# Kernel optimization log

Measured on AMD Instinct MI355X. Metric: run time of the kernel, lower is better.

The kernel has to match this reference:

```python
import jax, jax.numpy as jnp
import numpy as np

N = 100000      # nodes
E = 3200000     # edges
IN_DIM = 128
HID = 128
OUT_DIM = 1
LAYERS = 8
ALPHA = 0.1
THETA = 0.5


def setup_inputs() -> dict:
    key = jax.random.key(0)
    ks = jax.random.split(key, 8)
    x = jax.random.normal(ks[0], (N, IN_DIM), dtype=jnp.float32)
    edge_index = jax.random.randint(ks[1], (2, E), 0, N, dtype=jnp.int64)
    edge_weight = jax.random.uniform(ks[2], (E,), dtype=jnp.float32)  # unused by original forward path
    W_in = jax.random.normal(ks[3], (IN_DIM, HID), dtype=jnp.float32) * 0.05
    b_in = jnp.zeros((HID,), dtype=jnp.float32)
    W_gcn = jax.random.normal(ks[4], (LAYERS, HID, HID), dtype=jnp.float32) * 0.05
    W_out = jax.random.normal(ks[5], (HID, OUT_DIM), dtype=jnp.float32) * 0.05
    b_out = jnp.zeros((OUT_DIM,), dtype=jnp.float32)
    return {"x": x, "edge_weight": edge_weight, "W_in": W_in, "b_in": b_in,
            "W_gcn": W_gcn, "W_out": W_out, "b_out": b_out, "edge_index": edge_index}


def _gcn_norm(edge_index, dtype):
    # add self loops (fill value 1), symmetric normalization deg^-1/2 A deg^-1/2
    sl = jnp.arange(N, dtype=edge_index.dtype)
    row = jnp.concatenate([edge_index[0], sl])
    col = jnp.concatenate([edge_index[1], sl])
    w = jnp.ones(row.shape[0], dtype=dtype)
    deg = jax.ops.segment_sum(w, col, num_segments=N)
    dinv = jnp.where(deg > 0, jax.lax.rsqrt(deg), 0.0)
    norm = dinv[row] * dinv[col]
    return row, col, norm


def reference(x, edge_weight, W_in, b_in, W_gcn, W_out, b_out, edge_index):
    row, col, norm = _gcn_norm(edge_index, x.dtype)
    h = x @ W_in + b_in            # initial_proj
    h0 = h                          # residual x0
    for i in range(LAYERS):
        # dropout is identity in eval mode
        msg = h[row] * norm[:, None]                       # gather + scale [E+N, HID]
        agg = jax.ops.segment_sum(msg, col, num_segments=N)
        s = (1.0 - ALPHA) * agg + ALPHA * h0               # identity-mapped residual
        beta = float(np.log(THETA / (i + 1) + 1.0))
        h = (1.0 - beta) * s + beta * (s @ W_gcn[i])       # GCNII weight mix
        h = jax.nn.relu(h)
    return h @ W_out + b_out
```

## Files before the change

kernel.cpp:

```cpp
#include <hip/hip_runtime.h>
#include <hip/hip_bf16.h>
#include <math.h>

#define N_NODES 100000
#define N_EDGES 3200000
#define HID 128
#define LAYERS 8
#define ALPHA 0.1f
#define THETA 0.5f

#define SCAN_TILE 1024
#define NB_SCAN ((N_NODES + SCAN_TILE - 1) / SCAN_TILE)

typedef unsigned int uint;
typedef unsigned short ushort;
typedef __attribute__((ext_vector_type(8))) short short8;
typedef __attribute__((ext_vector_type(4))) float f32x4;

__device__ inline float bf_lo(uint p) { return __uint_as_float(p << 16); }
__device__ inline float bf_hi(uint p) { return __uint_as_float(p & 0xffff0000u); }
__device__ inline uint bf_pack(float x, float y) {
    uint ux = __float_as_uint(x), uy = __float_as_uint(y);
    uint rx = (ux + 0x7fffu + ((ux >> 16) & 1u)) >> 16;
    uint ry = (uy + 0x7fffu + ((uy >> 16) & 1u)) >> 16;
    return rx | (ry << 16);
}
__device__ inline ushort bfr(float x) {
    uint u = __float_as_uint(x);
    return (ushort)((u + 0x7fffu + ((u >> 16) & 1u)) >> 16);
}
__device__ inline float bff(ushort s) { return __uint_as_float(((uint)s) << 16); }

__device__ inline float rec_w(uint k) { return __uint_as_float((k >> 17) << 16); }

__global__ __launch_bounds__(256) void k_count(const int* __restrict__ col,
                                               int* __restrict__ cnt) {
    int e = blockIdx.x * 256 + threadIdx.x;
    if (e < N_EDGES) atomicAdd(&cnt[col[e]], 1);
}

__global__ __launch_bounds__(256) void k_dinv(const int* __restrict__ cnt,
                                              float* __restrict__ dinv) {
    int n = blockIdx.x * 256 + threadIdx.x;
    if (n < N_NODES) dinv[n] = rsqrtf((float)(cnt[n] + 1));
}

__global__ __launch_bounds__(256) void k_scan1(const int* __restrict__ cnt,
                                               int* __restrict__ indptr,
                                               int* __restrict__ bsum) {
    __shared__ int lds[256];
    int t = threadIdx.x;
    int base = blockIdx.x * SCAN_TILE + t * 4;
    int v[4];
    int s = 0;
#pragma unroll
    for (int j = 0; j < 4; ++j) {
        v[j] = (base + j < N_NODES) ? cnt[base + j] : 0;
        s += v[j];
    }
    lds[t] = s;
    __syncthreads();
    for (int off = 1; off < 256; off <<= 1) {
        int u = (t >= off) ? lds[t - off] : 0;
        __syncthreads();
        lds[t] += u;
        __syncthreads();
    }
    int run = lds[t] - s;
#pragma unroll
    for (int j = 0; j < 4; ++j) {
        if (base + j < N_NODES) indptr[base + j] = run;
        run += v[j];
    }
    if (t == 255) bsum[blockIdx.x] = lds[255];
}

__global__ __launch_bounds__(256) void k_scan2(const int* __restrict__ bsum,
                                               int* __restrict__ boff) {
    __shared__ int lds[256];
    int t = threadIdx.x;
    int v = (t < NB_SCAN) ? bsum[t] : 0;
    lds[t] = v;
    __syncthreads();
    for (int off = 1; off < 256; off <<= 1) {
        int u = (t >= off) ? lds[t - off] : 0;
        __syncthreads();
        lds[t] += u;
        __syncthreads();
    }
    boff[t] = lds[t] - v;
}

__global__ __launch_bounds__(256) void k_scan3(int* __restrict__ indptr,
                                               const int* __restrict__ boff) {
    int base = blockIdx.x * SCAN_TILE + threadIdx.x * 4;
    int add = boff[blockIdx.x];
#pragma unroll
    for (int j = 0; j < 4; ++j) {
        if (base + j < N_NODES) indptr[base + j] += add;
    }
    if (blockIdx.x == 0 && threadIdx.x == 0) indptr[N_NODES] = N_EDGES;
}

__global__ __launch_bounds__(256) void k_fill(const int* __restrict__ rowi,
                                              const int* __restrict__ coli,
                                              const float* __restrict__ dinv,
                                              const int* __restrict__ indptr,
                                              int* __restrict__ cursor,
                                              uint* __restrict__ csr4) {
    int e = blockIdx.x * 256 + threadIdx.x;
    if (e >= N_EDGES) return;
    int r = rowi[e];
    int c = coli[e];
    int p = indptr[c] + atomicAdd(&cursor[c], 1);
    float nrm = dinv[r] * dinv[c];
    csr4[p] = (uint)r | ((uint)bfr(nrm) << 17);
}

__global__ __launch_bounds__(256) void k_wprep(const float* __restrict__ Wg,
                                               ushort* __restrict__ Wt) {
    int l = blockIdx.x;
    const float* W = Wg + (size_t)l * HID * HID;
    ushort* T = Wt + (size_t)l * HID * HID;
    int t = threadIdx.x;
#pragma unroll
    for (int i = 0; i < 16; ++i) {
        int idx = t + 256 * i;
        int k = idx >> 5;
        int c4 = idx & 31;
        float4 v = *(const float4*)(W + (size_t)k * HID + c4 * 4);
        T[(c4 * 4 + 0) * HID + k] = bfr(v.x);
        T[(c4 * 4 + 1) * HID + k] = bfr(v.y);
        T[(c4 * 4 + 2) * HID + k] = bfr(v.z);
        T[(c4 * 4 + 3) * HID + k] = bfr(v.w);
    }
}

#define TN 32
#define SAS 136

__global__ __launch_bounds__(256) void k_layer(const uint* __restrict__ h,
                                               const uint* __restrict__ h0,
                                               const float* __restrict__ dinv,
                                               const int* __restrict__ indptr,
                                               const uint* __restrict__ csr4,
                                               const ushort* __restrict__ Wt,
                                               uint* __restrict__ hOut,
                                               float beta) {
    __shared__ ushort sA[TN * SAS];
    int t = threadIdx.x;
    int lane = t & 63;
    int wv = t >> 6;
    int nb = blockIdx.x * TN;

    for (int i = 0; i < 8; ++i) {
        int row = wv * 8 + i;
        int node = nb + row;
        int beg = indptr[node];
        int end = indptr[node + 1];
        float di = dinv[node];
        uint hs = h[node * 64 + lane];
        uint h0v = h0[node * 64 + lane];
        float ax[8], ay[8];
#pragma unroll
        for (int j = 0; j < 8; ++j) { ax[j] = 0.f; ay[j] = 0.f; }
        int e = beg;
        for (; e + 16 <= end; e += 16) {
            uint kk[16];
#pragma unroll
            for (int j = 0; j < 16; ++j) kk[j] = csr4[e + j];
            uint p[16];
#pragma unroll
            for (int j = 0; j < 16; ++j) p[j] = h[(kk[j] & 0x1FFFF) * 64 + lane];
#pragma unroll
            for (int j = 0; j < 16; ++j) {
                float w = rec_w(kk[j]);
                ax[j & 7] = fmaf(w, bf_lo(p[j]), ax[j & 7]);
                ay[j & 7] = fmaf(w, bf_hi(p[j]), ay[j & 7]);
            }
        }
        for (; e < end; e += 4) {
            uint kk[4];
            float w[4];
#pragma unroll
            for (int j = 0; j < 4; ++j) {
                int idx = e + j;
                kk[j] = csr4[idx < end ? idx : beg];
                w[j] = (idx < end) ? rec_w(kk[j]) : 0.f;
            }
            uint p[4];
#pragma unroll
            for (int j = 0; j < 4; ++j) p[j] = h[(kk[j] & 0x1FFFF) * 64 + lane];
#pragma unroll
            for (int j = 0; j < 4; ++j) {
                ax[j] = fmaf(w[j], bf_lo(p[j]), ax[j]);
                ay[j] = fmaf(w[j], bf_hi(p[j]), ay[j]);
            }
        }
        float sum0 = ((ax[0] + ax[1]) + (ax[2] + ax[3])) + ((ax[4] + ax[5]) + (ax[6] + ax[7]));
        float sum1 = ((ay[0] + ay[1]) + (ay[2] + ay[3])) + ((ay[4] + ay[5]) + (ay[6] + ay[7]));
        float selfw = di * di;
        float rx = (1.0f - ALPHA) * fmaf(selfw, bf_lo(hs), sum0) + ALPHA * bf_lo(h0v);
        float ry = (1.0f - ALPHA) * fmaf(selfw, bf_hi(hs), sum1) + ALPHA * bf_hi(h0v);
        *((uint*)(sA + row * SAS) + lane) = bf_pack(rx, ry);
    }
    __syncthreads();

    int fr = lane & 15;
    int fq = lane >> 4;
    f32x4 acc[2][2] = {};
#pragma unroll
    for (int kc = 0; kc < 4; ++kc) {
        int kof = kc * 32 + fq * 8;
        short8 b0 = *(const short8*)(Wt + (size_t)(wv * 32 + fr) * HID + kof);
        short8 b1 = *(const short8*)(Wt + (size_t)(wv * 32 + 16 + fr) * HID + kof);
#pragma unroll
        for (int tm = 0; tm < 2; ++tm) {
            short8 a = *(const short8*)(sA + (tm * 16 + fr) * SAS + kof);
            acc[tm][0] = __builtin_amdgcn_mfma_f32_16x16x32_bf16(a, b0, acc[tm][0], 0, 0, 0);
            acc[tm][1] = __builtin_amdgcn_mfma_f32_16x16x32_bf16(a, b1, acc[tm][1], 0, 0, 0);
        }
    }
    __syncthreads();

    float ob = 1.0f - beta;
#pragma unroll
    for (int tm = 0; tm < 2; ++tm)
#pragma unroll
        for (int tn = 0; tn < 2; ++tn)
#pragma unroll
            for (int r = 0; r < 4; ++r) {
                int row = tm * 16 + fq * 4 + r;
                int col = wv * 32 + tn * 16 + fr;
                float sv = bff(sA[row * SAS + col]);
                float val = fmaxf(fmaf(ob, sv, beta * acc[tm][tn][r]), 0.f);
                sA[row * SAS + col] = bfr(val);
            }
    __syncthreads();
#pragma unroll
    for (int i = 0; i < 2; ++i) {
        int idx = t + 256 * i;
        int r = idx >> 4;
        int q = idx & 15;
        *(uint4*)(hOut + (size_t)(nb + r) * 64 + q * 4) =
            *(const uint4*)((const uint*)(sA + r * SAS) + q * 4);
    }
}

__global__ __launch_bounds__(256) void k_gemm_in(const float* __restrict__ A,
                                                 const float* __restrict__ W,
                                                 const float* __restrict__ bias,
                                                 uint* __restrict__ out0,
                                                 uint* __restrict__ out1) {
    __shared__ float sT[32 * 64];
    __shared__ float Ws[32 * 128];
    int t = threadIdx.x;
    int tr = t & 15;
    int tc = t >> 4;
    int rowBase = blockIdx.x * 64;
    float acc[4][8] = {};

    for (int ko = 0; ko < HID; ko += 32) {
#pragma unroll
        for (int pass = 0; pass < 2; ++pass) {
            int lin = t + 256 * pass;
            int r = lin >> 3;
            int kq = lin & 7;
            int ar = rowBase + r;
            if (ar >= N_NODES) ar = N_NODES - 1;
            float4 v = *(const float4*)(A + (size_t)ar * HID + ko + 4 * kq);
            sT[(4 * kq + 0) * 64 + r] = v.x;
            sT[(4 * kq + 1) * 64 + r] = v.y;
            sT[(4 * kq + 2) * 64 + r] = v.z;
            sT[(4 * kq + 3) * 64 + r] = v.w;
        }
#pragma unroll
        for (int pass = 0; pass < 4; ++pass) {
            int lin = t + 256 * pass;
            int k = lin >> 5;
            int c4 = lin & 31;
            *(float4*)&Ws[k * 128 + 4 * c4] =
                *(const float4*)(W + (size_t)(ko + k) * HID + 4 * c4);
        }
        __syncthreads();
#pragma unroll
        for (int k = 0; k < 32; ++k) {
            float4 a = *(const float4*)&sT[k * 64 + 4 * tr];
            float4 w0 = *(const float4*)&Ws[k * 128 + 8 * tc];
            float4 w1 = *(const float4*)&Ws[k * 128 + 8 * tc + 4];
            float av[4] = {a.x, a.y, a.z, a.w};
            float wv[8] = {w0.x, w0.y, w0.z, w0.w, w1.x, w1.y, w1.z, w1.w};
#pragma unroll
            for (int i = 0; i < 4; ++i)
#pragma unroll
                for (int j = 0; j < 8; ++j)
                    acc[i][j] = fmaf(av[i], wv[j], acc[i][j]);
        }
        __syncthreads();
    }

    int c0 = 8 * tc;
    float bb[8];
#pragma unroll
    for (int j = 0; j < 8; ++j) bb[j] = bias[c0 + j];
#pragma unroll
    for (int i = 0; i < 4; ++i) {
        int r = rowBase + 4 * tr + i;
        if (r >= N_NODES) break;
        float v[8];
#pragma unroll
        for (int j = 0; j < 8; ++j) v[j] = acc[i][j] + bb[j];
        uint4 o;
        o.x = bf_pack(v[0], v[1]);
        o.y = bf_pack(v[2], v[3]);
        o.z = bf_pack(v[4], v[5]);
        o.w = bf_pack(v[6], v[7]);
        *(uint4*)(out0 + (size_t)r * 64 + c0 / 2) = o;
        *(uint4*)(out1 + (size_t)r * 64 + c0 / 2) = o;
    }
}

__global__ __launch_bounds__(256) void k_out(const uint* __restrict__ h,
                                             const float* __restrict__ W_out,
                                             const float* __restrict__ b_out,
                                             float* __restrict__ out) {
    int node = blockIdx.x * 4 + (threadIdx.x >> 6);
    if (node >= N_NODES) return;
    int lane = threadIdx.x & 63;
    uint p = h[node * 64 + lane];
    float2 wv = *(const float2*)(W_out + lane * 2);
    float pr = bf_lo(p) * wv.x + bf_hi(p) * wv.y;
#pragma unroll
    for (int off = 32; off > 0; off >>= 1) pr += __shfl_down(pr, off);
    if (lane == 0) out[node] = pr + b_out[0];
}

extern "C" void kernel_launch(void* const* d_in, const int* in_sizes, int n_in,
                              void* d_out, int out_size, void* d_ws, size_t ws_size,
                              hipStream_t stream) {
    const float* x     = (const float*)d_in[0];
    const float* W_in  = (const float*)d_in[2];
    const float* b_in  = (const float*)d_in[3];
    const float* W_gcn = (const float*)d_in[4];
    const float* W_out = (const float*)d_in[5];
    const float* b_out = (const float*)d_in[6];
    const int*   ei    = (const int*)d_in[7];
    const int* rowi = ei;
    const int* coli = ei + N_EDGES;
    float* out = (float*)d_out;

    char* ws = (char*)d_ws;
    auto alloc = [&](size_t bytes) -> char* {
        char* p = ws;
        ws += (bytes + 255) & ~(size_t)255;
        return p;
    };
    int*    cnt     = (int*)   alloc((size_t)N_NODES * 4);
    float*  dinv    = (float*) alloc((size_t)N_NODES * 4);
    int*    indptr  = (int*)   alloc((size_t)(N_NODES + 1) * 4);
    int*    cursor  = (int*)   alloc((size_t)N_NODES * 4);
    int*    bsum    = (int*)   alloc(1024 * 4);
    int*    boff    = (int*)   alloc(1024 * 4);
    uint*   csr4    = (uint*)  alloc((size_t)N_EDGES * 4);
    ushort* Wt      = (ushort*)alloc((size_t)LAYERS * HID * HID * 2);
    uint*   hA      = (uint*)  alloc((size_t)N_NODES * 64 * 4);
    uint*   hB      = (uint*)  alloc((size_t)N_NODES * 64 * 4);
    uint*   h0      = (uint*)  alloc((size_t)N_NODES * 64 * 4);

    hipMemsetAsync(cnt, 0, (size_t)N_NODES * 4, stream);
    hipMemsetAsync(cursor, 0, (size_t)N_NODES * 4, stream);

    k_count<<<(N_EDGES + 255) / 256, 256, 0, stream>>>(coli, cnt);
    k_dinv<<<(N_NODES + 255) / 256, 256, 0, stream>>>(cnt, dinv);
    k_scan1<<<NB_SCAN, 256, 0, stream>>>(cnt, indptr, bsum);
    k_scan2<<<1, 256, 0, stream>>>(bsum, boff);
    k_scan3<<<NB_SCAN, 256, 0, stream>>>(indptr, boff);
    k_fill<<<(N_EDGES + 255) / 256, 256, 0, stream>>>(rowi, coli, dinv, indptr,
                                                      cursor, csr4);
    k_wprep<<<LAYERS, 256, 0, stream>>>(W_gcn, Wt);

    k_gemm_in<<<(N_NODES + 63) / 64, 256, 0, stream>>>(x, W_in, b_in, h0, hA);

    int layer_blocks = N_NODES / TN;
    for (int l = 0; l < LAYERS; ++l) {
        const uint* hin = (l & 1) ? hB : hA;
        uint* hout      = (l & 1) ? hA : hB;
        float beta = logf(THETA / (float)(l + 1) + 1.0f);
        k_layer<<<layer_blocks, 256, 0, stream>>>(hin, h0, dinv, indptr, csr4,
                                                  Wt + (size_t)l * HID * HID,
                                                  hout, beta);
    }
    k_out<<<(N_NODES + 3) / 4, 256, 0, stream>>>(hA, W_out, b_out, out);
}
```

Measured before the change: 1.621 ms.

## Bucket CSR edges by source-node range and gather chunk-by-chunk across a wave's nodes

The CSR fill now runs as 8 passes, each covering one range of 12,500 source nodes, so each destination's neighbor list is sorted by source chunk. Per-chunk boundaries are snapshotted into a new array. The layer kernel walks the chunks in order and processes all 8 of a wave's nodes within each chunk before moving on, so concurrent gathers from h hit a narrower address range and should reuse cache better. The cost is 8 extra full edge-list passes plus snapshots in preprocessing, and many short inner loops per node that use the 4-wide tail path instead of the previous 16-wide unrolled loop.

Measured after the change: 2.043 ms. +26.1%, slower.

```diff
diff --git a/kernel.cpp b/kernel.cpp
--- a/kernel.cpp
+++ b/kernel.cpp
@@ -8,6 +8,9 @@
 #define LAYERS 8
 #define ALPHA 0.1f
 #define THETA 0.5f
+
+#define CH 8
+#define CHDIV 12500
 
 #define SCAN_TILE 1024
 #define NB_SCAN ((N_NODES + SCAN_TILE - 1) / SCAN_TILE)
@@ -102,17 +105,24 @@
     if (blockIdx.x == 0 && threadIdx.x == 0) indptr[N_NODES] = N_EDGES;
 }
 
-__global__ __launch_bounds__(256) void k_fill(const int* __restrict__ rowi,
-                                              const int* __restrict__ coli,
-                                              const float* __restrict__ dinv,
-                                              const int* __restrict__ indptr,
-                                              int* __restrict__ cursor,
-                                              uint* __restrict__ csr4) {
+__global__ __launch_bounds__(256) void k_snap(const int* __restrict__ src,
+                                              int* __restrict__ dst) {
+    int n = blockIdx.x * 256 + threadIdx.x;
+    if (n < N_NODES) dst[n] = src[n];
+}
+
+__global__ __launch_bounds__(256) void k_fill_pass(const int* __restrict__ rowi,
+                                                   const int* __restrict__ coli,
+                                                   const float* __restrict__ dinv,
+                                                   int* __restrict__ cursor,
+                                                   uint* __restrict__ csr4,
+                                                   int lo, int hi) {
     int e = blockIdx.x * 256 + threadIdx.x;
     if (e >= N_EDGES) return;
     int r = rowi[e];
+    if (r < lo || r >= hi) return;
     int c = coli[e];
-    int p = indptr[c] + atomicAdd(&cursor[c], 1);
+    int p = atomicAdd(&cursor[c], 1);
     float nrm = dinv[r] * dinv[c];
     csr4[p] = (uint)r | ((uint)bfr(nrm) << 17);
 }
@@ -143,6 +153,7 @@
                                                const uint* __restrict__ h0,
                                                const float* __restrict__ dinv,
                                                const int* __restrict__ indptr,
+                                               const int* __restrict__ bnd,
                                                const uint* __restrict__ csr4,
                                                const ushort* __restrict__ Wt,
                                                uint* __restrict__ hOut,
@@ -152,57 +163,52 @@
     int lane = t & 63;
     int wv = t >> 6;
     int nb = blockIdx.x * TN;
-
+    int myN = nb + wv * 8;
+
+    int bend = bnd[(lane & 7) * N_NODES + myN + (lane >> 3)];
+    int ip0 = indptr[myN + (lane & 7)];
+
+    float accx[8] = {0.f, 0.f, 0.f, 0.f, 0.f, 0.f, 0.f, 0.f};
+    float accy[8] = {0.f, 0.f, 0.f, 0.f, 0.f, 0.f, 0.f, 0.f};
+
+    for (int p = 0; p < CH; ++p) {
+#pragma unroll
+        for (int i = 0; i < 8; ++i) {
+            int end = __builtin_amdgcn_readlane(bend, i * 8 + p);
+            int beg = (p == 0) ? __builtin_amdgcn_readlane(ip0, i)
+                               : __builtin_amdgcn_readlane(bend, i * 8 + p - 1);
+            for (int e = beg; e < end; e += 4) {
+                uint kk[4];
+                float w[4];
+#pragma unroll
+                for (int j = 0; j < 4; ++j) {
+                    int idx = e + j;
+                    kk[j] = csr4[idx < end ? idx : beg];
+                    w[j] = (idx < end) ? rec_w(kk[j]) : 0.f;
+                }
+                uint pv[4];
+#pragma unroll
+                for (int j = 0; j < 4; ++j)
+                    pv[j] = h[(kk[j] & 0x1FFFF) * 64 + lane];
+#pragma unroll
+                for (int j = 0; j < 4; ++j) {
+                    accx[i] = fmaf(w[j], bf_lo(pv[j]), accx[i]);
+                    accy[i] = fmaf(w[j], bf_hi(pv[j]), accy[i]);
+                }
+            }
+        }
+    }
+
+#pragma unroll
     for (int i = 0; i < 8; ++i) {
-        int row = wv * 8 + i;
-        int node = nb + row;
-        int beg = indptr[node];
-        int end = indptr[node + 1];
+        int node = myN + i;
         float di = dinv[node];
         uint hs = h[node * 64 + lane];
         uint h0v = h0[node * 64 + lane];
-        float ax[8], ay[8];
-#pragma unroll
-        for (int j = 0; j < 8; ++j) { ax[j] = 0.f; ay[j] = 0.f; }
-        int e = beg;
-        for (; e + 16 <= end; e += 16) {
-            uint kk[16];
-#pragma unroll
-            for (int j = 0; j < 16; ++j) kk[j] = csr4[e + j];
-            uint p[16];
-#pragma unroll
-            for (int j = 0; j < 16; ++j) p[j] = h[(kk[j] & 0x1FFFF) * 64 + lane];
-#pragma unroll
-            for (int j = 0; j < 16; ++j) {
-                float w = rec_w(kk[j]);
-                ax[j & 7] = fmaf(w, bf_lo(p[j]), ax[j & 7]);
-                ay[j & 7] = fmaf(w, bf_hi(p[j]), ay[j & 7]);
-            }
-        }
-        for (; e < end; e += 4) {
-            uint kk[4];
-            float w[4];
-#pragma unroll
-            for (int j = 0; j < 4; ++j) {
-                int idx = e + j;
-                kk[j] = csr4[idx < end ? idx : beg];
-                w[j] = (idx < end) ? rec_w(kk[j]) : 0.f;
-            }
-            uint p[4];
-#pragma unroll
-            for (int j = 0; j < 4; ++j) p[j] = h[(kk[j] & 0x1FFFF) * 64 + lane];
-#pragma unroll
-            for (int j = 0; j < 4; ++j) {
-                ax[j] = fmaf(w[j], bf_lo(p[j]), ax[j]);
-                ay[j] = fmaf(w[j], bf_hi(p[j]), ay[j]);
-            }
-        }
-        float sum0 = ((ax[0] + ax[1]) + (ax[2] + ax[3])) + ((ax[4] + ax[5]) + (ax[6] + ax[7]));
-        float sum1 = ((ay[0] + ay[1]) + (ay[2] + ay[3])) + ((ay[4] + ay[5]) + (ay[6] + ay[7]));
         float selfw = di * di;
-        float rx = (1.0f - ALPHA) * fmaf(selfw, bf_lo(hs), sum0) + ALPHA * bf_lo(h0v);
-        float ry = (1.0f - ALPHA) * fmaf(selfw, bf_hi(hs), sum1) + ALPHA * bf_hi(h0v);
-        *((uint*)(sA + row * SAS) + lane) = bf_pack(rx, ry);
+        float rx = (1.0f - ALPHA) * fmaf(selfw, bf_lo(hs), accx[i]) + ALPHA * bf_lo(h0v);
+        float ry = (1.0f - ALPHA) * fmaf(selfw, bf_hi(hs), accy[i]) + ALPHA * bf_hi(h0v);
+        *((uint*)(sA + (wv * 8 + i) * SAS) + lane) = bf_pack(rx, ry);
     }
     __syncthreads();
 
@@ -359,6 +365,7 @@
     float*  dinv    = (float*) alloc((size_t)N_NODES * 4);
     int*    indptr  = (int*)   alloc((size_t)(N_NODES + 1) * 4);
     int*    cursor  = (int*)   alloc((size_t)N_NODES * 4);
+    int*    bnd     = (int*)   alloc((size_t)CH * N_NODES * 4);
     int*    bsum    = (int*)   alloc(1024 * 4);
     int*    boff    = (int*)   alloc(1024 * 4);
     uint*   csr4    = (uint*)  alloc((size_t)N_EDGES * 4);
@@ -368,15 +375,22 @@
     uint*   h0      = (uint*)  alloc((size_t)N_NODES * 64 * 4);
 
     hipMemsetAsync(cnt, 0, (size_t)N_NODES * 4, stream);
-    hipMemsetAsync(cursor, 0, (size_t)N_NODES * 4, stream);
-
-    k_count<<<(N_EDGES + 255) / 256, 256, 0, stream>>>(coli, cnt);
-    k_dinv<<<(N_NODES + 255) / 256, 256, 0, stream>>>(cnt, dinv);
+
+    int nblk = (N_NODES + 255) / 256;
+    int eblk = (N_EDGES + 255) / 256;
+
+    k_count<<<eblk, 256, 0, stream>>>(coli, cnt);
+    k_dinv<<<nblk, 256, 0, stream>>>(cnt, dinv);
     k_scan1<<<NB_SCAN, 256, 0, stream>>>(cnt, indptr, bsum);
     k_scan2<<<1, 256, 0, stream>>>(bsum, boff);
     k_scan3<<<NB_SCAN, 256, 0, stream>>>(indptr, boff);
-    k_fill<<<(N_EDGES + 255) / 256, 256, 0, stream>>>(rowi, coli, dinv, indptr,
-                                                      cursor, csr4);
+
+    k_snap<<<nblk, 256, 0, stream>>>(indptr, cursor);
+    for (int p = 0; p < CH; ++p) {
+        k_fill_pass<<<eblk, 256, 0, stream>>>(rowi, coli, dinv, cursor, csr4,
+                                              p * CHDIV, (p + 1) * CHDIV);
+        k_snap<<<nblk, 256, 0, stream>>>(cursor, bnd + (size_t)p * N_NODES);
+    }
     k_wprep<<<LAYERS, 256, 0, stream>>>(W_gcn, Wt);
 
     k_gemm_in<<<(N_NODES + 63) / 64, 256, 0, stream>>>(x, W_in, b_in, h0, hA);
@@ -386,7 +400,8 @@
         const uint* hin = (l & 1) ? hB : hA;
         uint* hout      = (l & 1) ? hA : hB;
         float beta = logf(THETA / (float)(l + 1) + 1.0f);
-        k_layer<<<layer_blocks, 256, 0, stream>>>(hin, h0, dinv, indptr, csr4,
+        k_layer<<<layer_blocks, 256, 0, stream>>>(hin, h0, dinv, indptr, bnd,
+                                                  csr4,
                                                   Wt + (size_t)l * HID * HID,
                                                   hout, beta);
     }
```

## Build CSR via two-pass bucketed binning instead of per-edge global atomics

Applied to the files above, without the earlier changes.

Replaces the single CSR fill kernel, which did one global atomic per edge on per-node cursors and scattered randomly, with a two-level scheme. Edges are first binned into 128-node buckets, each split into 8 sub-streams to spread atomic contention. A per-bucket kernel then places edges using LDS atomics, so final CSR writes land in a localized range. This adds an extra pass over the edges, a single-block bucket scan and a 12.8MB staging buffer.

Result: slower. 1.825 ms (+12.6%).

```diff
diff --git a/kernel.cpp b/kernel.cpp
--- a/kernel.cpp
+++ b/kernel.cpp
@@ -11,6 +11,11 @@
 
 #define SCAN_TILE 1024
 #define NB_SCAN ((N_NODES + SCAN_TILE - 1) / SCAN_TILE)
+
+#define BKN 128
+#define NBK ((N_NODES + BKN - 1) / BKN)
+#define NSTR (NBK * 8)
+#define BPTS 25
 
 typedef unsigned int uint;
 typedef unsigned short ushort;
@@ -34,9 +39,13 @@
 __device__ inline float rec_w(uint k) { return __uint_as_float((k >> 17) << 16); }
 
 __global__ __launch_bounds__(256) void k_count(const int* __restrict__ col,
-                                               int* __restrict__ cnt) {
+                                               int* __restrict__ cnt,
+                                               int* __restrict__ bktcnt8) {
     int e = blockIdx.x * 256 + threadIdx.x;
-    if (e < N_EDGES) atomicAdd(&cnt[col[e]], 1);
+    if (e >= N_EDGES) return;
+    int c = col[e];
+    atomicAdd(&cnt[c], 1);
+    atomicAdd(&bktcnt8[(c >> 7) * 8 + (blockIdx.x & 7)], 1);
 }
 
 __global__ __launch_bounds__(256) void k_dinv(const int* __restrict__ cnt,
@@ -102,19 +111,74 @@
     if (blockIdx.x == 0 && threadIdx.x == 0) indptr[N_NODES] = N_EDGES;
 }
 
-__global__ __launch_bounds__(256) void k_fill(const int* __restrict__ rowi,
-                                              const int* __restrict__ coli,
-                                              const float* __restrict__ dinv,
-                                              const int* __restrict__ indptr,
-                                              int* __restrict__ cursor,
-                                              uint* __restrict__ csr4) {
+__global__ __launch_bounds__(256) void k_bscan(const int* __restrict__ bktcnt8,
+                                               int* __restrict__ bcur8,
+                                               int* __restrict__ bktptr8) {
+    __shared__ int lds[256];
+    int t = threadIdx.x;
+    int base = t * BPTS;
+    int v[BPTS];
+    int s = 0;
+#pragma unroll
+    for (int j = 0; j < BPTS; ++j) {
+        v[j] = (base + j < NSTR) ? bktcnt8[base + j] : 0;
+        s += v[j];
+    }
+    lds[t] = s;
+    __syncthreads();
+    for (int off = 1; off < 256; off <<= 1) {
+        int u = (t >= off) ? lds[t - off] : 0;
+        __syncthreads();
+        lds[t] += u;
+        __syncthreads();
+    }
+    int run = lds[t] - s;
+#pragma unroll
+    for (int j = 0; j < BPTS; ++j) {
+        if (base + j < NSTR) { bcur8[base + j] = run; bktptr8[base + j] = run; }
+        run += v[j];
+    }
+    if (t == 255) bktptr8[NSTR] = N_EDGES;
+}
+
+__global__ __launch_bounds__(256) void k_bin(const int* __restrict__ rowi,
+                                             const int* __restrict__ coli,
+                                             int* __restrict__ bcur8,
+                                             uint* __restrict__ binned) {
     int e = blockIdx.x * 256 + threadIdx.x;
     if (e >= N_EDGES) return;
     int r = rowi[e];
     int c = coli[e];
-    int p = indptr[c] + atomicAdd(&cursor[c], 1);
-    float nrm = dinv[r] * dinv[c];
-    csr4[p] = (uint)r | ((uint)bfr(nrm) << 17);
+    int s = (c >> 7) * 8 + (blockIdx.x & 7);
+    int p = atomicAdd(&bcur8[s], 1);
+    binned[p] = (uint)r | ((uint)(c & 127) << 17);
+}
+
+__global__ __launch_bounds__(256) void k_scatter(const uint* __restrict__ binned,
+                                                 const int* __restrict__ bktptr8,
+                                                 const int* __restrict__ indptr,
+                                                 const float* __restrict__ dinv,
+                                                 uint* __restrict__ csr4) {
+    __shared__ int cur[BKN];
+    int b = blockIdx.x;
+    int t = threadIdx.x;
+    int nb = b * BKN;
+    if (t < BKN) {
+        int node = nb + t;
+        cur[t] = (node < N_NODES) ? indptr[node] : 0;
+    }
+    __syncthreads();
+    int beg = bktptr8[b * 8];
+    int end = bktptr8[b * 8 + 8];
+    for (int i = beg + t; i < end; i += 256) {
+        uint rec = binned[i];
+        int r = rec & 0x1FFFF;
+        int coff = rec >> 17;
+        int c = nb + coff;
+        int p = atomicAdd(&cur[coff], 1);
+        float nrm = dinv[r] * dinv[c];
+        csr4[p] = (uint)r | ((uint)bfr(nrm) << 17);
+    }
 }
 
 __global__ __launch_bounds__(256) void k_wprep(const float* __restrict__ Wg,
@@ -358,9 +422,12 @@
     int*    cnt     = (int*)   alloc((size_t)N_NODES * 4);
     float*  dinv    = (float*) alloc((size_t)N_NODES * 4);
     int*    indptr  = (int*)   alloc((size_t)(N_NODES + 1) * 4);
-    int*    cursor  = (int*)   alloc((size_t)N_NODES * 4);
+    int*    bktcnt8 = (int*)   alloc((size_t)NSTR * 4);
+    int*    bcur8   = (int*)   alloc((size_t)NSTR * 4);
+    int*    bktptr8 = (int*)   alloc((size_t)(NSTR + 8) * 4);
     int*    bsum    = (int*)   alloc(1024 * 4);
     int*    boff    = (int*)   alloc(1024 * 4);
+    uint*   binned  = (uint*)  alloc((size_t)N_EDGES * 4);
     uint*   csr4    = (uint*)  alloc((size_t)N_EDGES * 4);
     ushort* Wt      = (ushort*)alloc((size_t)LAYERS * HID * HID * 2);
     uint*   hA      = (uint*)  alloc((size_t)N_NODES * 64 * 4);
@@ -368,15 +435,20 @@
     uint*   h0      = (uint*)  alloc((size_t)N_NODES * 64 * 4);
 
     hipMemsetAsync(cnt, 0, (size_t)N_NODES * 4, stream);
-    hipMemsetAsync(cursor, 0, (size_t)N_NODES * 4, stream);
-
-    k_count<<<(N_EDGES + 255) / 256, 256, 0, stream>>>(coli, cnt);
+    hipMemsetAsync(bktcnt8, 0, (size_t)NSTR * 4, stream);
+
+    int nblk = (N_NODES + 255) / 256;
+    int eblk = (N_EDGES + 255) / 256;
+    (void)nblk;
+
+    k_count<<<eblk, 256, 0, stream>>>(coli, cnt, bktcnt8);
     k_dinv<<<(N_NODES + 255) / 256, 256, 0, stream>>>(cnt, dinv);
     k_scan1<<<NB_SCAN, 256, 0, stream>>>(cnt, indptr, bsum);
     k_scan2<<<1, 256, 0, stream>>>(bsum, boff);
     k_scan3<<<NB_SCAN, 256, 0, stream>>>(indptr, boff);
-    k_fill<<<(N_EDGES + 255) / 256, 256, 0, stream>>>(rowi, coli, dinv, indptr,
-                                                      cursor, csr4);
+    k_bscan<<<1, 256, 0, stream>>>(bktcnt8, bcur8, bktptr8);
+    k_bin<<<eblk, 256, 0, stream>>>(rowi, coli, bcur8, binned);
+    k_scatter<<<NBK, 256, 0, stream>>>(binned, bktptr8, indptr, dinv, csr4);
     k_wprep<<<LAYERS, 256, 0, stream>>>(W_gcn, Wt);
 
     k_gemm_in<<<(N_NODES + 63) / 64, 256, 0, stream>>>(x, W_in, b_in, h0, hA);
```
